# Kernel tuning notes

Measured on AMD Instinct MI355X. Metric: run time of the kernel, lower is better.

The kernel has to match this reference:

```python
import jax, jax.numpy as jnp
import numpy as np

N_IN, N_OUT, GRID_SIZE = 2048, 2048, 8

def setup_inputs() -> dict:
    key = jax.random.key(0)
    k1, k2 = jax.random.split(key)
    x = jax.random.normal(k1, (4096, N_IN), dtype=jnp.float32)
    coef = 0.1 * jax.random.normal(k2, (N_IN, N_OUT, GRID_SIZE), dtype=jnp.float32)
    grid = jnp.linspace(-1.0, 1.0, GRID_SIZE).astype(jnp.float32)
    return {"x": x, "coef": coef, "grid": grid}

def reference(x, coef, grid):
    # basis: [B, n_in, grid_size] gaussian bumps around grid points
    basis = jnp.exp(-5.0 * (x[..., None] - grid[None, None, :]) ** 2)
    basis = basis / (jnp.sum(basis, axis=-1, keepdims=True) + 1e-8)
    # y_j = sum_i sum_k basis[b,i,k] * coef[i,j,k]
    out = jnp.einsum('bik,ijk->bj', basis, coef)
    return out
```

## Files before the change

kernel.cpp:

```cpp
#include <hip/hip_runtime.h>
#include <hip/hip_bf16.h>

#define BATCH   4096
#define NIN     2048
#define NOUT    2048
#define GS      8

typedef __attribute__((ext_vector_type(8))) short  bf16x8;
typedef __attribute__((ext_vector_type(4))) short  bf16x4;
typedef __attribute__((ext_vector_type(4))) float  f32x4;

__device__ __forceinline__ short f2bf(float f) {
    unsigned u = __builtin_bit_cast(unsigned, f);
    u += 0x7fffu + ((u >> 16) & 1u);
    return (short)(u >> 16);
}

__device__ __forceinline__ bf16x8 basis_bf16(float xv, const float* g) {
    const float KE = -7.2134752044448170f;
    float e[GS], s = 0.f;
#pragma unroll
    for (int k = 0; k < GS; ++k) {
        float t = xv - g[k];
        e[k] = __builtin_amdgcn_exp2f(t * t * KE);
        s += e[k];
    }
    float rn = __builtin_amdgcn_rcpf(s + 1e-8f);
    bf16x8 fr;
#pragma unroll
    for (int k = 0; k < GS; ++k) fr[k] = f2bf(e[k] * rn);
    return fr;
}

__device__ __forceinline__ void async16(const void* g, void* l) {
    __builtin_amdgcn_global_load_lds(
        (const __attribute__((address_space(1))) unsigned*)g,
        (__attribute__((address_space(3))) unsigned*)l, 16, 0, 0);
}

#define PREP_BLOCKS 2048
#define TB 64
#define TI 32

__global__ __launch_bounds__(256, 4)
void kan_prep_kernel(const float* __restrict__ x, const float* __restrict__ coef,
                     const float* __restrict__ grid,
                     short* __restrict__ A_ws, short* __restrict__ B_ws)
{
    const int t = threadIdx.x;

    for (int c = blockIdx.x; c < (NIN * NOUT * GS) / 4096; c += PREP_BLOCKS) {
        const float* src = coef + (size_t)c * 4096;
        short*       dst = B_ws + (size_t)c * 4096;
        f32x4 v[4];
#pragma unroll
        for (int j = 0; j < 4; ++j)
            v[j] = *(const f32x4*)(src + j * 1024 + t * 4);
#pragma unroll
        for (int j = 0; j < 4; ++j) {
            bf16x4 o;
#pragma unroll
            for (int k = 0; k < 4; ++k) o[k] = f2bf(v[j][k]);
            *(bf16x4*)(dst + j * 1024 + t * 4) = o;
        }
    }

    __shared__ float tile[TB][TI + 1];
    float g[GS];
#pragma unroll
    for (int k = 0; k < GS; ++k) g[k] = grid[k];

    for (int job = blockIdx.x; job < (NIN / TI) * (BATCH / TB); job += PREP_BLOCKS) {
        const int i0 = (job & (NIN / TI - 1)) * TI;
        const int b0 = (job / (NIN / TI)) * TB;
        __syncthreads();
#pragma unroll
        for (int p = 0; p < (TB * TI) / 256; ++p) {
            int idx = t + p * 256;
            int b_l = idx >> 5, i_l = idx & 31;
            tile[b_l][i_l] = x[(size_t)(b0 + b_l) * NIN + i0 + i_l];
        }
        __syncthreads();
#pragma unroll
        for (int it = 0; it < 8; ++it) {
            int b_l = (t & 31) + 32 * (it & 1);
            int i_l = (t >> 5) + 8 * (it >> 1);
            bf16x8 fr = basis_bf16(tile[b_l][i_l], g);
            *(bf16x8*)(A_ws + (size_t)(i0 + i_l) * (BATCH * GS)
                            + (size_t)(b0 + b_l) * GS) = fr;
        }
    }
}

__global__ __launch_bounds__(256, 2)
void kan_gemm_kernel(const short* __restrict__ A_ws, const short* __restrict__ B_ws,
                     float* __restrict__ out)
{
    __shared__ __align__(16) char As[16384];
    __shared__ __align__(16) char Bs[16384];

    const int t    = threadIdx.x;
    const int wave = t >> 6;
    const int lane = t & 63;
    const int l15  = lane & 15;
    const int quad = lane >> 4;
    const int wm = wave & 1, wn = wave >> 1;
    const int m_blk = blockIdx.x * 128, n_blk = blockIdx.y * 128;

    f32x4 acc[4][4];
#pragma unroll
    for (int a = 0; a < 4; ++a)
#pragma unroll
        for (int b = 0; b < 4; ++b)
            acc[a][b] = (f32x4){0.f, 0.f, 0.f, 0.f};

    const char* Abase = (const char*)A_ws + (size_t)m_blk * (GS * 2);
    const char* Bbase = (const char*)B_ws + (size_t)n_blk * (GS * 2);
    const size_t strideA = (size_t)BATCH * GS * 2;
    const size_t strideB = (size_t)NOUT  * GS * 2;

    int dma_off[4], dma_iloc[4], dma_rem[4];
#pragma unroll
    for (int j = 0; j < 4; ++j) {
        dma_off[j]  = j * 4096 + t * 16;
        dma_iloc[j] = dma_off[j] >> 11;
        dma_rem[j]  = dma_off[j] & 2047;
    }

    for (int i0 = 0; i0 < NIN; i0 += 8) {
#pragma unroll
        for (int j = 0; j < 4; ++j) {
            const size_t i = (size_t)(i0 + dma_iloc[j]);
            async16(Abase + i * strideA + dma_rem[j], As + dma_off[j]);
            async16(Bbase + i * strideB + dma_rem[j], Bs + dma_off[j]);
        }
        __syncthreads();

#pragma unroll
        for (int s = 0; s < 2; ++s) {
            const int iloc = s * 4 + quad;
            bf16x8 af[4], bf[4];
#pragma unroll
            for (int ms = 0; ms < 4; ++ms)
                af[ms] = *(const bf16x8*)(As + (size_t)(iloc * 128 + wm * 64 + ms * 16 + l15) * 16);
#pragma unroll
            for (int ns = 0; ns < 4; ++ns)
                bf[ns] = *(const bf16x8*)(Bs + (size_t)(iloc * 128 + wn * 64 + ns * 16 + l15) * 16);
#pragma unroll
            for (int ms = 0; ms < 4; ++ms)
#pragma unroll
                for (int ns = 0; ns < 4; ++ns)
                    acc[ms][ns] = __builtin_amdgcn_mfma_f32_16x16x32_bf16(
                        af[ms], bf[ns], acc[ms][ns], 0, 0, 0);
        }
        __syncthreads();
    }

    const int m_base = m_blk + wm * 64;
    const int n_base = n_blk + wn * 64;
#pragma unroll
    for (int ms = 0; ms < 4; ++ms)
#pragma unroll
        for (int ns = 0; ns < 4; ++ns) {
            const int col = n_base + ns * 16 + l15;
#pragma unroll
            for (int r = 0; r < 4; ++r) {
                const int row = m_base + ms * 16 + quad * 4 + r;
                out[(size_t)row * NOUT + col] = acc[ms][ns][r];
            }
        }
}

__global__ __launch_bounds__(256, 2)
void kan_fused_kernel(const float* __restrict__ x, const float* __restrict__ coef,
                      const float* __restrict__ grid, float* __restrict__ out)
{
    const int tid  = threadIdx.x;
    const int wave = tid >> 6;
    const int lane = tid & 63;
    const int l15  = lane & 15;
    const int quad = lane >> 4;
    const int m_base = blockIdx.x * 128 + (wave & 1) * 64;
    const int n_base = blockIdx.y * 128 + (wave >> 1) * 64;

    float g[GS];
#pragma unroll
    for (int k = 0; k < GS; ++k) g[k] = grid[k];

    f32x4 acc[4][4];
#pragma unroll
    for (int a = 0; a < 4; ++a)
#pragma unroll
        for (int b = 0; b < 4; ++b) acc[a][b] = (f32x4){0.f, 0.f, 0.f, 0.f};

    const float* xp = x + (size_t)(m_base + l15) * NIN + quad;
    const float* cp = coef + (size_t)quad * (NOUT * GS) + (size_t)(n_base + l15) * GS;

    for (int i0 = 0; i0 < NIN; i0 += 4) {
        f32x4 braw[4][2];
#pragma unroll
        for (int ns = 0; ns < 4; ++ns) {
            const float* p = cp + ns * (16 * GS);
            braw[ns][0] = *(const f32x4*)(p);
            braw[ns][1] = *(const f32x4*)(p + 4);
        }
        bf16x8 afrag[4];
#pragma unroll
        for (int ms = 0; ms < 4; ++ms)
            afrag[ms] = basis_bf16(xp[ms * 16 * NIN], g);
        bf16x8 bfrag[4];
#pragma unroll
        for (int ns = 0; ns < 4; ++ns) {
            bf16x8 fr;
#pragma unroll
            for (int k = 0; k < 4; ++k) { fr[k] = f2bf(braw[ns][0][k]); fr[k+4] = f2bf(braw[ns][1][k]); }
            bfrag[ns] = fr;
        }
#pragma unroll
        for (int ms = 0; ms < 4; ++ms)
#pragma unroll
            for (int ns = 0; ns < 4; ++ns)
                acc[ms][ns] = __builtin_amdgcn_mfma_f32_16x16x32_bf16(
                    afrag[ms], bfrag[ns], acc[ms][ns], 0, 0, 0);
        xp += 4;
        cp += 4 * (NOUT * GS);
    }
#pragma unroll
    for (int ms = 0; ms < 4; ++ms)
#pragma unroll
        for (int ns = 0; ns < 4; ++ns) {
            const int col = n_base + ns * 16 + l15;
#pragma unroll
            for (int r = 0; r < 4; ++r)
                out[(size_t)(m_base + ms * 16 + quad * 4 + r) * NOUT + col] = acc[ms][ns][r];
        }
}

extern "C" void kernel_launch(void* const* d_in, const int* in_sizes, int n_in,
                              void* d_out, int out_size, void* d_ws, size_t ws_size,
                              hipStream_t stream) {
    const float* x    = (const float*)d_in[0];
    const float* coef = (const float*)d_in[1];
    const float* grid = (const float*)d_in[2];
    float* out        = (float*)d_out;

    const size_t a_elems = (size_t)NIN * BATCH * GS;
    const size_t b_elems = (size_t)NIN * NOUT * GS;
    const size_t need    = (a_elems + b_elems) * sizeof(short);

    if (ws_size >= need) {
        short* A_ws = (short*)d_ws;
        short* B_ws = A_ws + a_elems;

        kan_prep_kernel<<<PREP_BLOCKS, 256, 0, stream>>>(x, coef, grid, A_ws, B_ws);

        dim3 g2(BATCH / 128, NOUT / 128);
        kan_gemm_kernel<<<g2, 256, 0, stream>>>(A_ws, B_ws, out);
    } else {
        dim3 grd(BATCH / 128, NOUT / 128);
        kan_fused_kernel<<<grd, 256, 0, stream>>>(x, coef, grid, out);
    }
}
```

Before: 541.6 us.

## Add split-K GEMM with partial-sum reduction and tune prep kernel

Splits the reduction over input features into two halves across a third grid dimension, writes each half's result to a workspace partial buffer, and sums the halves in a separate reduce kernel. Occupancy for the GEMM is raised to 4 blocks per SM. The prep kernel also doubles its block count and uses nontemporal loads for coef. Doubling the number of GEMM blocks is meant to fill the GPU better, at the cost of 64 MB of extra partial-result writes and reads plus an extra launch, and it needs a larger workspace.

```diff
diff --git a/kernel.cpp b/kernel.cpp
--- a/kernel.cpp
+++ b/kernel.cpp
@@ -38,7 +38,7 @@
         (__attribute__((address_space(3))) unsigned*)l, 16, 0, 0);
 }
 
-#define PREP_BLOCKS 2048
+#define PREP_BLOCKS 4096
 #define TB 64
 #define TI 32
 
@@ -55,7 +55,7 @@
         f32x4 v[4];
 #pragma unroll
         for (int j = 0; j < 4; ++j)
-            v[j] = *(const f32x4*)(src + j * 1024 + t * 4);
+            v[j] = __builtin_nontemporal_load((const f32x4*)(src + j * 1024 + t * 4));
 #pragma unroll
         for (int j = 0; j < 4; ++j) {
             bf16x4 o;
@@ -92,9 +92,9 @@
     }
 }
 
-__global__ __launch_bounds__(256, 2)
-void kan_gemm_kernel(const short* __restrict__ A_ws, const short* __restrict__ B_ws,
-                     float* __restrict__ out)
+__global__ __launch_bounds__(256, 4)
+void kan_gemm_splitk(const short* __restrict__ A_ws, const short* __restrict__ B_ws,
+                     float* __restrict__ P)
 {
     __shared__ __align__(16) char As[16384];
     __shared__ __align__(16) char Bs[16384];
@@ -106,6 +106,7 @@
     const int quad = lane >> 4;
     const int wm = wave & 1, wn = wave >> 1;
     const int m_blk = blockIdx.x * 128, n_blk = blockIdx.y * 128;
+    const int z = blockIdx.z;
 
     f32x4 acc[4][4];
 #pragma unroll
@@ -127,7 +128,8 @@
         dma_rem[j]  = dma_off[j] & 2047;
     }
 
-    for (int i0 = 0; i0 < NIN; i0 += 8) {
+    const int i_lo = z * (NIN / 2), i_hi = i_lo + (NIN / 2);
+    for (int i0 = i_lo; i0 < i_hi; i0 += 8) {
 #pragma unroll
         for (int j = 0; j < 4; ++j) {
             const size_t i = (size_t)(i0 + dma_iloc[j]);
@@ -136,6 +138,97 @@
         }
         __syncthreads();
 
+#pragma unroll
+        for (int s = 0; s < 2; ++s) {
+            const int iloc = s * 4 + quad;
+            bf16x8 af[4], bf[4];
+#pragma unroll
+            for (int ms = 0; ms < 4; ++ms)
+                af[ms] = *(const bf16x8*)(As + (size_t)(iloc * 128 + wm * 64 + ms * 16 + l15) * 16);
+#pragma unroll
+            for (int ns = 0; ns < 4; ++ns)
+                bf[ns] = *(const bf16x8*)(Bs + (size_t)(iloc * 128 + wn * 64 + ns * 16 + l15) * 16);
+#pragma unroll
+            for (int ms = 0; ms < 4; ++ms)
+#pragma unroll
+                for (int ns = 0; ns < 4; ++ns)
+                    acc[ms][ns] = __builtin_amdgcn_mfma_f32_16x16x32_bf16(
+                        af[ms], bf[ns], acc[ms][ns], 0, 0, 0);
+        }
+        __syncthreads();
+    }
+
+    float* Pz = P + (size_t)z * ((size_t)BATCH * NOUT);
+    const int m_base = m_blk + wm * 64;
+    const int n_base = n_blk + wn * 64;
+#pragma unroll
+    for (int ms = 0; ms < 4; ++ms)
+#pragma unroll
+        for (int ns = 0; ns < 4; ++ns) {
+            const int col = n_base + ns * 16 + l15;
+#pragma unroll
+            for (int r = 0; r < 4; ++r) {
+                const int row = m_base + ms * 16 + quad * 4 + r;
+                Pz[(size_t)row * NOUT + col] = acc[ms][ns][r];
+            }
+        }
+}
+
+__global__ __launch_bounds__(256, 4)
+void kan_reduce_kernel(const float* __restrict__ P, float* __restrict__ out)
+{
+    const size_t n4 = (size_t)BATCH * NOUT / 4;
+    for (size_t idx = (size_t)blockIdx.x * 256 + threadIdx.x; idx < n4;
+         idx += (size_t)1024 * 256) {
+        f32x4 a = ((const f32x4*)P)[idx];
+        f32x4 b = ((const f32x4*)P)[idx + n4];
+        ((f32x4*)out)[idx] = a + b;
+    }
+}
+
+__global__ __launch_bounds__(256, 2)
+void kan_gemm_kernel(const short* __restrict__ A_ws, const short* __restrict__ B_ws,
+                     float* __restrict__ out)
+{
+    __shared__ __align__(16) char As[16384];
+    __shared__ __align__(16) char Bs[16384];
+
+    const int t    = threadIdx.x;
+    const int wave = t >> 6;
+    const int lane = t & 63;
+    const int l15  = lane & 15;
+    const int quad = lane >> 4;
+    const int wm = wave & 1, wn = wave >> 1;
+    const int m_blk = blockIdx.x * 128, n_blk = blockIdx.y * 128;
+
+    f32x4 acc[4][4];
+#pragma unroll
+    for (int a = 0; a < 4; ++a)
+#pragma unroll
+        for (int b = 0; b < 4; ++b)
+            acc[a][b] = (f32x4){0.f, 0.f, 0.f, 0.f};
+
+    const char* Abase = (const char*)A_ws + (size_t)m_blk * (GS * 2);
+    const char* Bbase = (const char*)B_ws + (size_t)n_blk * (GS * 2);
+    const size_t strideA = (size_t)BATCH * GS * 2;
+    const size_t strideB = (size_t)NOUT  * GS * 2;
+
+    int dma_off[4], dma_iloc[4], dma_rem[4];
+#pragma unroll
+    for (int j = 0; j < 4; ++j) {
+        dma_off[j]  = j * 4096 + t * 16;
+        dma_iloc[j] = dma_off[j] >> 11;
+        dma_rem[j]  = dma_off[j] & 2047;
+    }
+
+    for (int i0 = 0; i0 < NIN; i0 += 8) {
+#pragma unroll
+        for (int j = 0; j < 4; ++j) {
+            const size_t i = (size_t)(i0 + dma_iloc[j]);
+            async16(Abase + i * strideA + dma_rem[j], As + dma_off[j]);
+            async16(Bbase + i * strideB + dma_rem[j], Bs + dma_off[j]);
+        }
+        __syncthreads();
 #pragma unroll
         for (int s = 0; s < 2; ++s) {
             const int iloc = s * 4 + quad;
@@ -246,16 +339,25 @@
 
     const size_t a_elems = (size_t)NIN * BATCH * GS;
     const size_t b_elems = (size_t)NIN * NOUT * GS;
-    const size_t need    = (a_elems + b_elems) * sizeof(short);
-
-    if (ws_size >= need) {
+    const size_t p_elems = (size_t)2 * BATCH * NOUT;
+    const size_t need_basic  = (a_elems + b_elems) * sizeof(short);
+    const size_t need_splitk = need_basic + p_elems * sizeof(float);
+
+    if (ws_size >= need_basic) {
         short* A_ws = (short*)d_ws;
         short* B_ws = A_ws + a_elems;
 
         kan_prep_kernel<<<PREP_BLOCKS, 256, 0, stream>>>(x, coef, grid, A_ws, B_ws);
 
-        dim3 g2(BATCH / 128, NOUT / 128);
-        kan_gemm_kernel<<<g2, 256, 0, stream>>>(A_ws, B_ws, out);
+        if (ws_size >= need_splitk) {
+            float* P = (float*)(B_ws + b_elems);
+            dim3 g2(BATCH / 128, NOUT / 128, 2);
+            kan_gemm_splitk<<<g2, 256, 0, stream>>>(A_ws, B_ws, P);
+            kan_reduce_kernel<<<1024, 256, 0, stream>>>(P, out);
+        } else {
+            dim3 g2(BATCH / 128, NOUT / 128);
+            kan_gemm_kernel<<<g2, 256, 0, stream>>>(A_ws, B_ws, out);
+        }
     } else {
         dim3 grd(BATCH / 128, NOUT / 128);
         kan_fused_kernel<<<grd, 256, 0, stream>>>(x, coef, grid, out);
```

Result: faster. 498.8 us (-7.9%).
